# Performance work log

Hardware: AMD Instinct MI355X
Metric: run time of the kernel (lower is better)

## Reference

```python
import jax, jax.numpy as jnp
import numpy as np

B, S, D = 4, 2048, 1024
NH, HD = 16, 64  # num_heads, head_dim; NH*HD == D


def setup_inputs() -> dict:
    key = jax.random.key(0)
    ks = jax.random.split(key, 10)
    s = 0.02
    return {
        "x": jax.random.normal(ks[0], (B, S, D), dtype=jnp.float32),
        "attention_mask": jnp.zeros((B, 1, 1, S), dtype=jnp.float32),
        "Wq": jax.random.normal(ks[1], (D, D), dtype=jnp.float32) * s,
        "bq": jnp.zeros((D,), dtype=jnp.float32),
        "Wk": jax.random.normal(ks[2], (D, D), dtype=jnp.float32) * s,
        "bk": jnp.zeros((D,), dtype=jnp.float32),
        "Wv": jax.random.normal(ks[3], (D, D), dtype=jnp.float32) * s,
        "bv": jnp.zeros((D,), dtype=jnp.float32),
        "Wo": jax.random.normal(ks[4], (D, D), dtype=jnp.float32) * s,
        "bo": jnp.zeros((D,), dtype=jnp.float32),
    }


def _heads(t):
    # [B,S,D] -> [B,NH,S,HD]
    return t.reshape(B, S, NH, HD).transpose(0, 2, 1, 3)


def reference(x, attention_mask, Wq, bq, Wk, bk, Wv, bv, Wo, bo):
    q = _heads(x @ Wq + bq)
    k = _heads(x @ Wk + bk)
    v = _heads(x @ Wv + bv)
    scores = jnp.einsum("bhqd,bhkd->bhqk", q, k) / jnp.sqrt(jnp.float32(HD))
    scores = scores + attention_mask
    attn = jax.nn.softmax(scores, axis=-1)  # dropout p=0 -> identity
    ctx = jnp.einsum("bhqk,bhkd->bhqd", attn, v)
    ctx = ctx.transpose(0, 2, 1, 3).reshape(B, S, D)
    return ctx @ Wo + bo
```

## Files before the change

### kernel.cpp

```cpp
#include <hip/hip_runtime.h>
#include <cstdint>
#include <cstddef>

typedef unsigned short u16;
typedef __attribute__((ext_vector_type(8))) __bf16 bf16x8;
typedef __attribute__((ext_vector_type(4))) float f32x4;
typedef __attribute__((ext_vector_type(16))) float f32x16;
typedef __attribute__((ext_vector_type(2))) uint32_t u32x2;
typedef __attribute__((ext_vector_type(4))) float float4v;

#define BATCH 4
#define S_LEN 2048
#define DMODEL 1024
#define NHEAD 16
#define HDIM 64
#define MROWS (BATCH * S_LEN)
#define LOG2E 1.4426950408889634f
#define SC_L (0.125f * LOG2E)

__device__ __forceinline__ u16 f2bf(float f) {
  uint32_t u = __float_as_uint(f);
  u += 0x7fffu + ((u >> 16) & 1u);
  return (u16)(u >> 16);
}

#if __has_builtin(__builtin_amdgcn_cvt_pk_bf16_f32)
__device__ __forceinline__ uint32_t packbf2(float a, float b) {
  auto t = __builtin_amdgcn_cvt_pk_bf16_f32(a, b);
  uint32_t u;
  __builtin_memcpy(&u, &t, 4);
  return u;
}
#else
__device__ __forceinline__ uint32_t packbf2(float a, float b) {
  uint32_t ua = __float_as_uint(a) + 0x8000u;
  uint32_t ub = __float_as_uint(b) + 0x8000u;
  return (ub & 0xFFFF0000u) | (ua >> 16);
}
#endif

#if __has_builtin(__builtin_amdgcn_exp2f)
#define EXP2(x) __builtin_amdgcn_exp2f(x)
#else
#define EXP2(x) exp2f(x)
#endif

typedef __attribute__((address_space(1))) void gvoid_t;
typedef __attribute__((address_space(3))) void svoid_t;
__device__ __forceinline__ void gl_lds16(const void* g, void* s) {
  __builtin_amdgcn_global_load_lds((gvoid_t*)g, (svoid_t*)s, 16, 0, 0);
}

__global__ __launch_bounds__(256) void cvt4_kernel(const float4v* __restrict__ in,
                                                   u32x2* __restrict__ out, int n4) {
  int i = blockIdx.x * blockDim.x + threadIdx.x;
  if (i < n4) {
    float4v v = in[i];
    u32x2 o;
    o.x = packbf2(v.x, v.y);
    o.y = packbf2(v.z, v.w);
    out[i] = o;
  }
}

__global__ __launch_bounds__(256) void maskl_kernel(const float* __restrict__ in,
                                                    float* __restrict__ out, int n) {
  int i = blockIdx.x * blockDim.x + threadIdx.x;
  if (i < n) out[i] = in[i] * LOG2E;
}

__global__ __launch_bounds__(256) void tcvt_kernel(const float* __restrict__ W0,
                                                   const float* __restrict__ W1,
                                                   const float* __restrict__ W2,
                                                   const float* __restrict__ W3,
                                                   u16* __restrict__ Wall) {
  __shared__ float tile[32][33];
  const int z = blockIdx.z;
  const float* W = (z == 0) ? W0 : (z == 1) ? W1 : (z == 2) ? W2 : W3;
  u16* Wt = Wall + (size_t)z * DMODEL * DMODEL;
  const int n0 = blockIdx.x * 32, k0 = blockIdx.y * 32;
  const int x = threadIdx.x, y = threadIdx.y;
  for (int yy = y; yy < 32; yy += 8)
    tile[yy][x] = W[(size_t)(k0 + yy) * DMODEL + n0 + x];
  __syncthreads();
  for (int yy = y; yy < 32; yy += 8)
    Wt[(size_t)(n0 + yy) * DMODEL + k0 + x] = f2bf(tile[x][yy]);
}

template <int MODE>
__global__ __launch_bounds__(256) void gemm128(const u16* __restrict__ A,
                                               const u16* __restrict__ Bt,
                                               const float* __restrict__ b0,
                                               const float* __restrict__ b1,
                                               const float* __restrict__ b2,
                                               void* __restrict__ o0,
                                               void* __restrict__ o1,
                                               void* __restrict__ o2) {
  __shared__ u16 As[128 * 32];
  __shared__ u16 Bs[128 * 32];
  const int tid = threadIdx.x;
  const int wid = tid >> 6;
  const int lane = tid & 63;
  const int l16 = lane & 15;
  const int g4 = lane >> 4;
  const int m0 = blockIdx.x * 128;
  const int n0 = blockIdx.y * 128;
  const int wm = (wid & 1) * 64;
  const int wn = (wid >> 1) * 64;

  const int srow = tid >> 2;
  const int sk = (tid & 3) * 8;
  const u16* gA = A + (size_t)(m0 + srow) * DMODEL + sk;
  const u16* gB = Bt + (size_t)(n0 + srow) * DMODEL + sk;
  char* sA = (char*)As + wid * 1024;
  char* sB = (char*)Bs + wid * 1024;

  f32x4 acc[4][4];
#pragma unroll
  for (int i = 0; i < 4; ++i)
#pragma unroll
    for (int j = 0; j < 4; ++j) acc[i][j] = (f32x4){0.f, 0.f, 0.f, 0.f};

  for (int k0 = 0; k0 < DMODEL; k0 += 32) {
    __syncthreads();
    gl_lds16(gA + k0, sA);
    gl_lds16(gA + (size_t)64 * DMODEL + k0, sA + 4096);
    gl_lds16(gB + k0, sB);
    gl_lds16(gB + (size_t)64 * DMODEL + k0, sB + 4096);
    __syncthreads();

    bf16x8 af[4], bfr[4];
#pragma unroll
    for (int i = 0; i < 4; ++i)
      af[i] = *(const bf16x8*)(As + (wm + i * 16 + l16) * 32 + g4 * 8);
#pragma unroll
    for (int j = 0; j < 4; ++j)
      bfr[j] = *(const bf16x8*)(Bs + (wn + j * 16 + l16) * 32 + g4 * 8);
#pragma unroll
    for (int i = 0; i < 4; ++i)
#pragma unroll
      for (int j = 0; j < 4; ++j)
        acc[i][j] = __builtin_amdgcn_mfma_f32_16x16x32_bf16(af[i], bfr[j],
                                                            acc[i][j], 0, 0, 0);
  }

  const int seg = n0 >> 10;
  const float* bp = (MODE == 1 || seg == 0) ? b0 : (seg == 1 ? b1 : b2);
  void* op = (MODE == 1 || seg == 0) ? o0 : (seg == 1 ? o1 : o2);

#pragma unroll
  for (int i = 0; i < 4; ++i) {
#pragma unroll
    for (int j = 0; j < 4; ++j) {
      const int coll = n0 + wn + j * 16 + l16;
      const int cseg = coll & 1023;
      const float bval = bp[cseg];
#pragma unroll
      for (int r = 0; r < 4; ++r) {
        const int rowg = m0 + wm + i * 16 + g4 * 4 + r;
        const float v = acc[i][j][r] + bval;
        if (MODE == 0) {
          const int b = rowg >> 11, s = rowg & (S_LEN - 1);
          const int h = cseg >> 6, d = cseg & (HDIM - 1);
          if (seg == 2) {
            ((u16*)op)[(((size_t)(b * NHEAD + h) * HDIM + d) << 11) + s] = f2bf(v);
          } else {
            ((u16*)op)[((size_t)((b * NHEAD + h) * S_LEN + s) << 6) + d] = f2bf(v);
          }
        } else {
          ((float*)op)[(size_t)rowg * DMODEL + cseg] = v;
        }
      }
    }
  }
}

__global__ __launch_bounds__(256, 2) void attn4_kernel(const u16* __restrict__ Q,
                                                       const u16* __restrict__ K,
                                                       const u16* __restrict__ Vt,
                                                       const float* __restrict__ maskL,
                                                       u16* __restrict__ ctx) {
  __shared__ u16 Ks[64 * 72];
  __shared__ u16 Vs[64 * 72];

  const int tid = threadIdx.x;
  const int wid = tid >> 6;
  const int lane = tid & 63;
  const int l32 = lane & 31;
  const int hi = lane >> 5;
  const int flat = blockIdx.y * gridDim.x + blockIdx.x;
  const int nf = (flat & 7) * 64 + (flat >> 3);
  const int bx = nf & 7;
  const int bh = nf >> 3;
  const int b = bh >> 4;
  const int h = bh & 15;
  const int qw0 = bx * 256 + wid * 64;

  const u16* Qbase = Q + (size_t)bh * S_LEN * HDIM;
  bf16x8 aq[2][4];
#pragma unroll
  for (int qh = 0; qh < 2; ++qh)
#pragma unroll
    for (int c = 0; c < 4; ++c)
      aq[qh][c] = *(const bf16x8*)(Qbase + (size_t)(qw0 + qh * 32 + l32) * HDIM +
                                   c * 16 + hi * 8);

  union { u16 s[8]; bf16x8 v; } onesu;
#pragma unroll
  for (int i = 0; i < 8; ++i) onesu.s[i] = 0x3F80;
  const bf16x8 onesv = onesu.v;

  const f32x16 z16 = {};
  f32x16 oacc[2][2] = {};
  f32x16 lacc[2] = {};

  const int srow = tid >> 3;
  const int scol = (tid & 7) * 8;
  const int keyg = scol >> 4;
  const int todd = (scol >> 3) & 1;
  const int vkb = keyg * 16 + todd * 4;
  const u16* Kg = K + (size_t)bh * S_LEN * HDIM + (size_t)srow * HDIM + scol;
  const u16* Vg = Vt + (size_t)bh * HDIM * S_LEN + (size_t)srow * S_LEN + scol;
  const float* mrow = maskL + (size_t)b * S_LEN;

  for (int kt = 0; kt < S_LEN; kt += 64) {
    bf16x8 kv0 = *(const bf16x8*)(Kg + (size_t)kt * HDIM);
    bf16x8 kv1 = *(const bf16x8*)(Kg + (size_t)(kt + 32) * HDIM);
    union { bf16x8 v; uint32_t u[4]; } vv0, vv1;
    vv0.v = *(const bf16x8*)(Vg + kt);
    vv1.v = *(const bf16x8*)(Vg + (size_t)32 * S_LEN + kt);
    __syncthreads();
    *(bf16x8*)(Ks + srow * 72 + scol) = kv0;
    *(bf16x8*)(Ks + (srow + 32) * 72 + scol) = kv1;
    *(u32x2*)(Vs + srow * 72 + vkb) = (u32x2){vv0.u[0], vv0.u[1]};
    *(u32x2*)(Vs + srow * 72 + vkb + 8) = (u32x2){vv0.u[2], vv0.u[3]};
    *(u32x2*)(Vs + (srow + 32) * 72 + vkb) = (u32x2){vv1.u[0], vv1.u[1]};
    *(u32x2*)(Vs + (srow + 32) * 72 + vkb + 8) = (u32x2){vv1.u[2], vv1.u[3]};
    __syncthreads();

    uint32_t P[2][2][8];
#pragma unroll
    for (int T = 0; T < 2; ++T) {
      bf16x8 kf[4];
#pragma unroll
      for (int c = 0; c < 4; ++c)
        kf[c] = *(const bf16x8*)(Ks + (T * 32 + l32) * 72 + c * 16 + hi * 8);
      f32x4 m4[4];
#pragma unroll
      for (int tq = 0; tq < 4; ++tq)
        m4[tq] = *(const f32x4*)(mrow + kt + T * 32 + tq * 8 + hi * 4);
#pragma unroll
      for (int qh = 0; qh < 2; ++qh) {
        f32x16 s = __builtin_amdgcn_mfma_f32_32x32x16_bf16(kf[0], aq[qh][0], z16, 0, 0, 0);
#pragma unroll
        for (int c = 1; c < 4; ++c)
          s = __builtin_amdgcn_mfma_f32_32x32x16_bf16(kf[c], aq[qh][c], s, 0, 0, 0);
#pragma unroll
        for (int tq = 0; tq < 4; ++tq) {
          float p0 = EXP2(fmaf(s[tq * 4 + 0], SC_L, m4[tq][0]));
          float p1 = EXP2(fmaf(s[tq * 4 + 1], SC_L, m4[tq][1]));
          float p2 = EXP2(fmaf(s[tq * 4 + 2], SC_L, m4[tq][2]));
          float p3 = EXP2(fmaf(s[tq * 4 + 3], SC_L, m4[tq][3]));
          P[T][qh][tq * 2] = packbf2(p0, p1);
          P[T][qh][tq * 2 + 1] = packbf2(p2, p3);
        }
      }
    }

#pragma unroll
    for (int c = 0; c < 4; ++c) {
      const int T = c >> 1, half = c & 1;
      bf16x8 vf[2];
#pragma unroll
      for (int dh = 0; dh < 2; ++dh)
        vf[dh] = *(const bf16x8*)(Vs + (dh * 32 + l32) * 72 + c * 16 + hi * 8);
#pragma unroll
      for (int qh = 0; qh < 2; ++qh) {
        union { uint32_t u[4]; bf16x8 v; } pf;
#pragma unroll
        for (int e = 0; e < 4; ++e) pf.u[e] = P[T][qh][half * 4 + e];
        oacc[qh][0] = __builtin_amdgcn_mfma_f32_32x32x16_bf16(pf.v, vf[0], oacc[qh][0], 0, 0, 0);
        oacc[qh][1] = __builtin_amdgcn_mfma_f32_32x32x16_bf16(pf.v, vf[1], oacc[qh][1], 0, 0, 0);
        lacc[qh] = __builtin_amdgcn_mfma_f32_32x32x16_bf16(pf.v, onesv, lacc[qh], 0, 0, 0);
      }
    }
  }

#pragma unroll
  for (int qh = 0; qh < 2; ++qh) {
#pragma unroll
    for (int reg = 0; reg < 16; ++reg) {
      const int q = qw0 + qh * 32 + (reg & 3) + 8 * (reg >> 2) + 4 * hi;
      const float inv = 1.0f / lacc[qh][reg];
      u16* cp = ctx + ((size_t)(b * S_LEN + q) * NHEAD + h) * HDIM;
      cp[l32] = f2bf(oacc[qh][0][reg] * inv);
      cp[32 + l32] = f2bf(oacc[qh][1][reg] * inv);
    }
  }
}

extern "C" void kernel_launch(void* const* d_in, const int* in_sizes, int n_in,
                              void* d_out, int out_size, void* d_ws, size_t ws_size,
                              hipStream_t stream) {
  const float* x = (const float*)d_in[0];
  const float* mask = (const float*)d_in[1];
  const float* Wq = (const float*)d_in[2];
  const float* bq = (const float*)d_in[3];
  const float* Wk = (const float*)d_in[4];
  const float* bk = (const float*)d_in[5];
  const float* Wv = (const float*)d_in[6];
  const float* bv = (const float*)d_in[7];
  const float* Wo = (const float*)d_in[8];
  const float* bo = (const float*)d_in[9];
  float* out = (float*)d_out;

  char* ws = (char*)d_ws;
  size_t off = 0;
  u16* xb = (u16*)(ws + off);    off += (size_t)MROWS * DMODEL * 2;
  u16* wall = (u16*)(ws + off);  off += (size_t)4 * DMODEL * DMODEL * 2;
  u16* Qh = (u16*)(ws + off);    off += (size_t)MROWS * DMODEL * 2;
  u16* Kh = (u16*)(ws + off);    off += (size_t)MROWS * DMODEL * 2;
  u16* Vtb = (u16*)(ws + off);   off += (size_t)MROWS * DMODEL * 2;
  u16* ctxb = (u16*)(ws + off);  off += (size_t)MROWS * DMODEL * 2;
  float* mL = (float*)(ws + off); off += (size_t)BATCH * S_LEN * 4;
  (void)ws_size; (void)in_sizes; (void)n_in; (void)out_size;

  const int nx4 = MROWS * DMODEL / 4;
  cvt4_kernel<<<dim3(nx4 / 256), dim3(256), 0, stream>>>((const float4v*)x, (u32x2*)xb, nx4);
  maskl_kernel<<<dim3(BATCH * S_LEN / 256), dim3(256), 0, stream>>>(mask, mL, BATCH * S_LEN);
  tcvt_kernel<<<dim3(32, 32, 4), dim3(32, 8), 0, stream>>>(Wq, Wk, Wv, Wo, wall);

  gemm128<0><<<dim3(MROWS / 128, 3 * DMODEL / 128), dim3(256), 0, stream>>>(
      xb, wall, bq, bk, bv, (void*)Qh, (void*)Kh, (void*)Vtb);

  attn4_kernel<<<dim3(S_LEN / 256, BATCH * NHEAD), dim3(256), 0, stream>>>(Qh, Kh, Vtb, mL, ctxb);

  gemm128<1><<<dim3(MROWS / 128, DMODEL / 128), dim3(256), 0, stream>>>(
      ctxb, wall + (size_t)3 * DMODEL * DMODEL, bo, bo, bo, (void*)out, (void*)out, (void*)out);
}
```

Before: 296.7 us.

## Restructure attention tiling, stage V-transpose writes through LDS, fuse prep kernels

The attention kernel now gives each wave 32 queries instead of 64 and processes 128-key tiles per iteration. The row sum is accumulated with scalar adds and a shuffle instead of an extra MFMA against a ones vector, and launch bounds ask for 4 blocks per SM. The QKV GEMM epilogue for V now transposes tiles through shared memory so the transposed V store uses 16-byte vector writes instead of scattered 2-byte writes. The x conversion and mask scaling kernels are merged into one launch. Together these target fewer MFMAs, more latency hiding through occupancy, better store coalescing and less launch overhead, at the cost of less Q reuse per K/V tile and more register pressure.

```diff
diff --git a/kernel.cpp b/kernel.cpp
--- a/kernel.cpp
+++ b/kernel.cpp
@@ -51,22 +51,25 @@
   __builtin_amdgcn_global_load_lds((gvoid_t*)g, (svoid_t*)s, 16, 0, 0);
 }
 
-__global__ __launch_bounds__(256) void cvt4_kernel(const float4v* __restrict__ in,
-                                                   u32x2* __restrict__ out, int n4) {
+__global__ __launch_bounds__(256) void prep_kernel(const float4v* __restrict__ x,
+                                                   u32x2* __restrict__ xb,
+                                                   const float4v* __restrict__ mask,
+                                                   float4v* __restrict__ mL,
+                                                   int nx4, int nm4) {
   int i = blockIdx.x * blockDim.x + threadIdx.x;
-  if (i < n4) {
-    float4v v = in[i];
+  if (i < nx4) {
+    float4v v = x[i];
     u32x2 o;
     o.x = packbf2(v.x, v.y);
     o.y = packbf2(v.z, v.w);
-    out[i] = o;
-  }
-}
-
-__global__ __launch_bounds__(256) void maskl_kernel(const float* __restrict__ in,
-                                                    float* __restrict__ out, int n) {
-  int i = blockIdx.x * blockDim.x + threadIdx.x;
-  if (i < n) out[i] = in[i] * LOG2E;
+    xb[i] = o;
+  } else {
+    int j = i - nx4;
+    if (j < nm4) {
+      float4v m = mask[j];
+      mL[j] = m * LOG2E;
+    }
+  }
 }
 
 __global__ __launch_bounds__(256) void tcvt_kernel(const float* __restrict__ W0,
@@ -148,6 +151,35 @@
   const float* bp = (MODE == 1 || seg == 0) ? b0 : (seg == 1 ? b1 : b2);
   void* op = (MODE == 1 || seg == 0) ? o0 : (seg == 1 ? o1 : o2);
 
+  if (MODE == 0 && seg == 2) {
+    __syncthreads();
+    u16* Tr = ((wid & 2) ? Bs : As) + (wid & 1) * 1152;
+#pragma unroll
+    for (int j = 0; j < 4; ++j) {
+      const int cseg = (n0 + wn + j * 16 + l16) & 1023;
+      const float bval = bp[cseg];
+#pragma unroll
+      for (int i = 0; i < 4; ++i) {
+        u32x2 w;
+        w.x = packbf2(acc[i][j][0] + bval, acc[i][j][1] + bval);
+        w.y = packbf2(acc[i][j][2] + bval, acc[i][j][3] + bval);
+        *(u32x2*)(Tr + l16 * 72 + i * 16 + g4 * 4) = w;
+      }
+#pragma unroll
+      for (int rr = 0; rr < 2; ++rr) {
+        const int n_loc = rr * 8 + (lane >> 3);
+        const int m_loc = (lane & 7) * 8;
+        bf16x8 v = *(const bf16x8*)(Tr + n_loc * 72 + m_loc);
+        const int cs2 = (n0 + wn + j * 16 + n_loc) & 1023;
+        const int h = cs2 >> 6, d = cs2 & 63;
+        const int mg = m0 + wm + m_loc;
+        const int b = mg >> 11, s = mg & (S_LEN - 1);
+        *(bf16x8*)((u16*)op + (((size_t)(b * NHEAD + h) * HDIM + d) << 11) + s) = v;
+      }
+    }
+    return;
+  }
+
 #pragma unroll
   for (int i = 0; i < 4; ++i) {
 #pragma unroll
@@ -162,11 +194,7 @@
         if (MODE == 0) {
           const int b = rowg >> 11, s = rowg & (S_LEN - 1);
           const int h = cseg >> 6, d = cseg & (HDIM - 1);
-          if (seg == 2) {
-            ((u16*)op)[(((size_t)(b * NHEAD + h) * HDIM + d) << 11) + s] = f2bf(v);
-          } else {
-            ((u16*)op)[((size_t)((b * NHEAD + h) * S_LEN + s) << 6) + d] = f2bf(v);
-          }
+          ((u16*)op)[((size_t)((b * NHEAD + h) * S_LEN + s) << 6) + d] = f2bf(v);
         } else {
           ((float*)op)[(size_t)rowg * DMODEL + cseg] = v;
         }
@@ -175,13 +203,13 @@
   }
 }
 
-__global__ __launch_bounds__(256, 2) void attn4_kernel(const u16* __restrict__ Q,
+__global__ __launch_bounds__(256, 4) void attn5_kernel(const u16* __restrict__ Q,
                                                        const u16* __restrict__ K,
                                                        const u16* __restrict__ Vt,
                                                        const float* __restrict__ maskL,
                                                        u16* __restrict__ ctx) {
-  __shared__ u16 Ks[64 * 72];
-  __shared__ u16 Vs[64 * 72];
+  __shared__ u16 Ks[128 * 72];
+  __shared__ u16 Vs[64 * 136];
 
   const int tid = threadIdx.x;
   const int wid = tid >> 6;
@@ -189,113 +217,93 @@
   const int l32 = lane & 31;
   const int hi = lane >> 5;
   const int flat = blockIdx.y * gridDim.x + blockIdx.x;
-  const int nf = (flat & 7) * 64 + (flat >> 3);
-  const int bx = nf & 7;
-  const int bh = nf >> 3;
+  const int nf = (flat & 7) * 128 + (flat >> 3);
+  const int bx = nf & 15;
+  const int bh = nf >> 4;
   const int b = bh >> 4;
   const int h = bh & 15;
-  const int qw0 = bx * 256 + wid * 64;
-
-  const u16* Qbase = Q + (size_t)bh * S_LEN * HDIM;
-  bf16x8 aq[2][4];
-#pragma unroll
-  for (int qh = 0; qh < 2; ++qh)
-#pragma unroll
-    for (int c = 0; c < 4; ++c)
-      aq[qh][c] = *(const bf16x8*)(Qbase + (size_t)(qw0 + qh * 32 + l32) * HDIM +
-                                   c * 16 + hi * 8);
-
-  union { u16 s[8]; bf16x8 v; } onesu;
-#pragma unroll
-  for (int i = 0; i < 8; ++i) onesu.s[i] = 0x3F80;
-  const bf16x8 onesv = onesu.v;
+  const int q0w = bx * 128 + wid * 32;
+
+  const u16* Qp = Q + ((size_t)bh * S_LEN + q0w + l32) * HDIM;
+  bf16x8 aq[4];
+#pragma unroll
+  for (int c = 0; c < 4; ++c)
+    aq[c] = *(const bf16x8*)(Qp + c * 16 + hi * 8);
 
   const f32x16 z16 = {};
-  f32x16 oacc[2][2] = {};
-  f32x16 lacc[2] = {};
-
-  const int srow = tid >> 3;
-  const int scol = (tid & 7) * 8;
-  const int keyg = scol >> 4;
-  const int todd = (scol >> 3) & 1;
-  const int vkb = keyg * 16 + todd * 4;
-  const u16* Kg = K + (size_t)bh * S_LEN * HDIM + (size_t)srow * HDIM + scol;
-  const u16* Vg = Vt + (size_t)bh * HDIM * S_LEN + (size_t)srow * S_LEN + scol;
+  f32x16 oacc[2] = {};
+  float lsum = 0.f;
+
+  const int krow = tid >> 1;
+  const int kcol = (tid & 1) * 32;
+  const int vd = tid >> 2;
+  const int vc = (tid & 3) * 32;
+  const u16* Kg = K + (size_t)bh * S_LEN * HDIM + (size_t)krow * HDIM + kcol;
+  const u16* Vg = Vt + (size_t)bh * HDIM * S_LEN + (size_t)vd * S_LEN + vc;
   const float* mrow = maskL + (size_t)b * S_LEN;
 
-  for (int kt = 0; kt < S_LEN; kt += 64) {
-    bf16x8 kv0 = *(const bf16x8*)(Kg + (size_t)kt * HDIM);
-    bf16x8 kv1 = *(const bf16x8*)(Kg + (size_t)(kt + 32) * HDIM);
-    union { bf16x8 v; uint32_t u[4]; } vv0, vv1;
-    vv0.v = *(const bf16x8*)(Vg + kt);
-    vv1.v = *(const bf16x8*)(Vg + (size_t)32 * S_LEN + kt);
-    __syncthreads();
-    *(bf16x8*)(Ks + srow * 72 + scol) = kv0;
-    *(bf16x8*)(Ks + (srow + 32) * 72 + scol) = kv1;
-    *(u32x2*)(Vs + srow * 72 + vkb) = (u32x2){vv0.u[0], vv0.u[1]};
-    *(u32x2*)(Vs + srow * 72 + vkb + 8) = (u32x2){vv0.u[2], vv0.u[3]};
-    *(u32x2*)(Vs + (srow + 32) * 72 + vkb) = (u32x2){vv1.u[0], vv1.u[1]};
-    *(u32x2*)(Vs + (srow + 32) * 72 + vkb + 8) = (u32x2){vv1.u[2], vv1.u[3]};
-    __syncthreads();
-
-    uint32_t P[2][2][8];
-#pragma unroll
-    for (int T = 0; T < 2; ++T) {
+  for (int kt = 0; kt < S_LEN; kt += 128) {
+    bf16x8 kv[4];
+    union { bf16x8 v; uint32_t u[4]; } vv[4];
+#pragma unroll
+    for (int r = 0; r < 4; ++r) {
+      kv[r] = *(const bf16x8*)(Kg + (size_t)kt * HDIM + r * 8);
+      vv[r].v = *(const bf16x8*)(Vg + kt + r * 8);
+    }
+    __syncthreads();
+#pragma unroll
+    for (int r = 0; r < 4; ++r) {
+      *(bf16x8*)(Ks + krow * 72 + kcol + r * 8) = kv[r];
+      const int kb = vc + r * 8;
+      const int vkb = ((kb >> 4) << 4) + (((kb >> 3) & 1) << 2);
+      *(u32x2*)(Vs + vd * 136 + vkb) = (u32x2){vv[r].u[0], vv[r].u[1]};
+      *(u32x2*)(Vs + vd * 136 + vkb + 8) = (u32x2){vv[r].u[2], vv[r].u[3]};
+    }
+    __syncthreads();
+
+    union PU { uint32_t u[8]; bf16x8 v[2]; } P[4];
+#pragma unroll
+    for (int T = 0; T < 4; ++T) {
       bf16x8 kf[4];
 #pragma unroll
       for (int c = 0; c < 4; ++c)
         kf[c] = *(const bf16x8*)(Ks + (T * 32 + l32) * 72 + c * 16 + hi * 8);
-      f32x4 m4[4];
-#pragma unroll
-      for (int tq = 0; tq < 4; ++tq)
-        m4[tq] = *(const f32x4*)(mrow + kt + T * 32 + tq * 8 + hi * 4);
-#pragma unroll
-      for (int qh = 0; qh < 2; ++qh) {
-        f32x16 s = __builtin_amdgcn_mfma_f32_32x32x16_bf16(kf[0], aq[qh][0], z16, 0, 0, 0);
-#pragma unroll
-        for (int c = 1; c < 4; ++c)
-          s = __builtin_amdgcn_mfma_f32_32x32x16_bf16(kf[c], aq[qh][c], s, 0, 0, 0);
-#pragma unroll
-        for (int tq = 0; tq < 4; ++tq) {
-          float p0 = EXP2(fmaf(s[tq * 4 + 0], SC_L, m4[tq][0]));
-          float p1 = EXP2(fmaf(s[tq * 4 + 1], SC_L, m4[tq][1]));
-          float p2 = EXP2(fmaf(s[tq * 4 + 2], SC_L, m4[tq][2]));
-          float p3 = EXP2(fmaf(s[tq * 4 + 3], SC_L, m4[tq][3]));
-          P[T][qh][tq * 2] = packbf2(p0, p1);
-          P[T][qh][tq * 2 + 1] = packbf2(p2, p3);
-        }
+      f32x16 s = __builtin_amdgcn_mfma_f32_32x32x16_bf16(kf[0], aq[0], z16, 0, 0, 0);
+#pragma unroll
+      for (int c = 1; c < 4; ++c)
+        s = __builtin_amdgcn_mfma_f32_32x32x16_bf16(kf[c], aq[c], s, 0, 0, 0);
+#pragma unroll
+      for (int tq = 0; tq < 4; ++tq) {
+        f32x4 m4 = *(const f32x4*)(mrow + kt + T * 32 + tq * 8 + hi * 4);
+        float p0 = EXP2(fmaf(s[tq * 4 + 0], SC_L, m4[0]));
+        float p1 = EXP2(fmaf(s[tq * 4 + 1], SC_L, m4[1]));
+        float p2 = EXP2(fmaf(s[tq * 4 + 2], SC_L, m4[2]));
+        float p3 = EXP2(fmaf(s[tq * 4 + 3], SC_L, m4[3]));
+        lsum += (p0 + p1) + (p2 + p3);
+        P[T].u[tq * 2] = packbf2(p0, p1);
+        P[T].u[tq * 2 + 1] = packbf2(p2, p3);
       }
     }
 
 #pragma unroll
-    for (int c = 0; c < 4; ++c) {
-      const int T = c >> 1, half = c & 1;
-      bf16x8 vf[2];
-#pragma unroll
-      for (int dh = 0; dh < 2; ++dh)
-        vf[dh] = *(const bf16x8*)(Vs + (dh * 32 + l32) * 72 + c * 16 + hi * 8);
-#pragma unroll
-      for (int qh = 0; qh < 2; ++qh) {
-        union { uint32_t u[4]; bf16x8 v; } pf;
-#pragma unroll
-        for (int e = 0; e < 4; ++e) pf.u[e] = P[T][qh][half * 4 + e];
-        oacc[qh][0] = __builtin_amdgcn_mfma_f32_32x32x16_bf16(pf.v, vf[0], oacc[qh][0], 0, 0, 0);
-        oacc[qh][1] = __builtin_amdgcn_mfma_f32_32x32x16_bf16(pf.v, vf[1], oacc[qh][1], 0, 0, 0);
-        lacc[qh] = __builtin_amdgcn_mfma_f32_32x32x16_bf16(pf.v, onesv, lacc[qh], 0, 0, 0);
-      }
-    }
-  }
-
-#pragma unroll
-  for (int qh = 0; qh < 2; ++qh) {
-#pragma unroll
-    for (int reg = 0; reg < 16; ++reg) {
-      const int q = qw0 + qh * 32 + (reg & 3) + 8 * (reg >> 2) + 4 * hi;
-      const float inv = 1.0f / lacc[qh][reg];
-      u16* cp = ctx + ((size_t)(b * S_LEN + q) * NHEAD + h) * HDIM;
-      cp[l32] = f2bf(oacc[qh][0][reg] * inv);
-      cp[32 + l32] = f2bf(oacc[qh][1][reg] * inv);
-    }
+    for (int c = 0; c < 8; ++c) {
+      bf16x8 pf = P[c >> 1].v[c & 1];
+      bf16x8 vf0 = *(const bf16x8*)(Vs + l32 * 136 + c * 16 + hi * 8);
+      bf16x8 vf1 = *(const bf16x8*)(Vs + (32 + l32) * 136 + c * 16 + hi * 8);
+      oacc[0] = __builtin_amdgcn_mfma_f32_32x32x16_bf16(pf, vf0, oacc[0], 0, 0, 0);
+      oacc[1] = __builtin_amdgcn_mfma_f32_32x32x16_bf16(pf, vf1, oacc[1], 0, 0, 0);
+    }
+  }
+
+  const float lc = lsum + __shfl_xor(lsum, 32);
+#pragma unroll
+  for (int reg = 0; reg < 16; ++reg) {
+    const int qt = (reg & 3) + 8 * (reg >> 2) + 4 * hi;
+    const float inv = 1.0f / __shfl(lc, qt, 32);
+    const int q = q0w + qt;
+    u16* cp = ctx + ((size_t)(b * S_LEN + q) * NHEAD + h) * HDIM;
+    cp[l32] = f2bf(oacc[0][reg] * inv);
+    cp[32 + l32] = f2bf(oacc[1][reg] * inv);
   }
 }
 
@@ -326,14 +334,15 @@
   (void)ws_size; (void)in_sizes; (void)n_in; (void)out_size;
 
   const int nx4 = MROWS * DMODEL / 4;
-  cvt4_kernel<<<dim3(nx4 / 256), dim3(256), 0, stream>>>((const float4v*)x, (u32x2*)xb, nx4);
-  maskl_kernel<<<dim3(BATCH * S_LEN / 256), dim3(256), 0, stream>>>(mask, mL, BATCH * S_LEN);
+  const int nm4 = BATCH * S_LEN / 4;
+  prep_kernel<<<dim3((nx4 + nm4 + 255) / 256), dim3(256), 0, stream>>>(
+      (const float4v*)x, (u32x2*)xb, (const float4v*)mask, (float4v*)mL, nx4, nm4);
   tcvt_kernel<<<dim3(32, 32, 4), dim3(32, 8), 0, stream>>>(Wq, Wk, Wv, Wo, wall);
 
   gemm128<0><<<dim3(MROWS / 128, 3 * DMODEL / 128), dim3(256), 0, stream>>>(
       xb, wall, bq, bk, bv, (void*)Qh, (void*)Kh, (void*)Vtb);
 
-  attn4_kernel<<<dim3(S_LEN / 256, BATCH * NHEAD), dim3(256), 0, stream>>>(Qh, Kh, Vtb, mL, ctxb);
+  attn5_kernel<<<dim3(S_LEN / 128, BATCH * NHEAD), dim3(256), 0, stream>>>(Qh, Kh, Vtb, mL, ctxb);
 
   gemm128<1><<<dim3(MROWS / 128, DMODEL / 128), dim3(256), 0, stream>>>(
       ctxb, wall + (size_t)3 * DMODEL * DMODEL, bo, bo, bo, (void*)out, (void*)out, (void*)out);
```

Result: slower. 304.8 us (+2.7%).
